# Optimization experiments

Hardware: AMD Instinct MI355X
Metric: run time of the kernel (lower is better)

Reference implementation:

```python
import jax, jax.numpy as jnp
import numpy as np

N, R, H, OUT = 512, 16, 16, 1
EPSILON = 1e-6
CUTOFF = 5.0  # ExpNormalSmearing cutoff_upper (cutoff_lower = 0)


def exp_normal_smearing(dist):
    # dist: (N, N, 1) -> (N, N, R); TorchMD-Net style ExpNormalSmearing
    start = jnp.exp(-CUTOFF)
    means = jnp.linspace(start, 1.0, R, dtype=dist.dtype)
    beta = (2.0 / R * (1.0 - start)) ** -2
    cutoff = 0.5 * (jnp.cos(dist * jnp.pi / CUTOFF) + 1.0) * (dist < CUTOFF)
    return cutoff * jnp.exp(-beta * (jnp.exp(-dist) - means) ** 2)


def setup_inputs() -> dict:
    key = jax.random.key(0)
    ks = jax.random.split(key, 9)
    s_in = 1.0 / np.sqrt(H * H)
    s_h = 1.0 / np.sqrt(H)
    return {
        "x": jax.random.normal(ks[0], (N, 3), jnp.float32) * 1.5,
        "W": jax.random.normal(ks[1], (2, N, R, H), jnp.float32) * 0.1,
        "W1": jax.random.normal(ks[2], (H, H * H), jnp.float32) * s_in,
        "b1": jax.random.normal(ks[3], (H,), jnp.float32) * 0.01,
        "W2": jax.random.normal(ks[4], (4 * R * H, H), jnp.float32) * s_h,
        "W3": jax.random.normal(ks[5], (H, H * H), jnp.float32) * s_in,
        "b3": jax.random.normal(ks[6], (H,), jnp.float32) * 0.01,
        "W4": jax.random.normal(ks[7], (OUT, H), jnp.float32) * s_h,
        "b4": jax.random.normal(ks[8], (OUT,), jnp.float32) * 0.01,
    }


def reference(x, W, W1, b1, W2, W3, b3, W4, b4):
    K, Q = W[0], W[1]                               # (N, R, H) each
    diff = x[:, None, :] - x[None, :, :]            # (N, N, 3)
    nsq = jnp.sum(diff * diff, axis=-1, keepdims=True) + EPSILON
    norm = jnp.sqrt(nsq)                            # (N, N, 1)
    diff = diff / nsq                               # note: divided by squared norm (faithful)
    sm = exp_normal_smearing(norm)                  # (N, N, R)
    basis = sm[..., None] * diff[..., None, :]      # (N, N, R, 3)

    bk = jnp.einsum('ijrb,jrc->icb', basis, K)      # (N, H, 3)
    bq = jnp.einsum('ijrb,jrc->icb', basis, Q)
    att = jnp.einsum('ihb,igb->ihg', bk, bq).reshape(N, H * H)
    att = jax.nn.silu(att @ W1.T + b1) @ W2.T       # (N, 4*R*H), second Linear bias-free

    left, right = att[:, : 2 * R * H], att[:, 2 * R * H:]
    pair = left[:, None, :] + right[None, :, :]     # (N, N, 2*R*H)
    K2 = pair[..., : R * H].reshape(N, N, R, H)
    Q2 = pair[..., R * H:].reshape(N, N, R, H)

    bk = jnp.einsum('ijrb,ijrc->icb', basis, K2)    # (N, H, 3)
    bq = jnp.einsum('ijrb,ijrc->icb', basis, Q2)
    att = jnp.einsum('ihb,igb->ihg', bk, bq).reshape(N, H * H)
    return jax.nn.silu(att @ W3.T + b3) @ W4.T + b4  # (N, OUT)
```

## Files before the change

### kernel.cpp

```cpp
#include <hip/hip_runtime.h>
#include <hip/hip_bf16.h>
#include <math.h>

#define NN 512

#define START 0.006737946999085467f
#define STEP  ((1.0f - START) * (1.0f/15.0f))
#define SB    (0.125f * (1.0f - START))
#define BETA  (1.0f/(SB*SB))
#define LOG2E 1.4426950408889634f
#define NB    (-(BETA)*LOG2E)


__global__ __launch_bounds__(256) void k0(const float* __restrict__ W,
                                          float* __restrict__ Wt)
{
    __shared__ float ldsb[256];
    const int row = blockIdx.x;
    ldsb[threadIdx.x] = W[(size_t)row*256 + threadIdx.x];
    __syncthreads();
    const int c = threadIdx.x >> 4, r = threadIdx.x & 15;
    Wt[(size_t)row*256 + threadIdx.x] = ldsb[r*16 + c];
}

__global__ __launch_bounds__(256) void k1a(const float* __restrict__ x,
                                           const float* __restrict__ Wt,
                                           float* __restrict__ part1)
{
    const int ib = blockIdx.x & 127, jc = blockIdx.x >> 7;
    const int i0 = ib * 4;
    const int tid = threadIdx.x;
    const int c = tid & 15, js = tid >> 4;
    const int lane = tid & 63, wv = tid >> 6;

    __shared__ float  lG[4][64][16];
    __shared__ float4 lP[4][64];
    __shared__ float  s_part[4][16][26];

    {
        const int pi = tid >> 6, pj = tid & 63;
        const int jg = jc*64 + pj;
        const float xi0 = x[(i0+pi)*3+0], xi1 = x[(i0+pi)*3+1], xi2 = x[(i0+pi)*3+2];
        float d0 = xi0 - x[jg*3+0];
        float d1 = xi1 - x[jg*3+1];
        float d2 = xi2 - x[jg*3+2];
        float nsq = fmaf(d0,d0, fmaf(d1,d1, fmaf(d2,d2, 1e-6f)));
        float rs  = __builtin_amdgcn_rsqf(nsq);
        float nrm = nsq * rs;
        float inv = rs * rs;
        float cutv = 0.f;
        if (nrm < 5.0f) cutv = 0.5f*(__cosf(nrm*0.6283185307179586f)+1.0f);
        float en = exp2f(-LOG2E * nrm);
        lP[pi][pj] = make_float4(d0*inv, d1*inv, d2*inv, 0.f);
        float4* dst = reinterpret_cast<float4*>(&lG[pi][pj][0]);
        #pragma unroll
        for (int rq = 0; rq < 4; ++rq) {
            float t0 = en - (START + STEP*(float)(4*rq+0));
            float t1 = en - (START + STEP*(float)(4*rq+1));
            float t2 = en - (START + STEP*(float)(4*rq+2));
            float t3 = en - (START + STEP*(float)(4*rq+3));
            dst[rq] = make_float4(cutv*exp2f(NB*t0*t0), cutv*exp2f(NB*t1*t1),
                                  cutv*exp2f(NB*t2*t2), cutv*exp2f(NB*t3*t3));
        }
    }
    __syncthreads();

    float acc[24];
    #pragma unroll
    for (int v = 0; v < 24; ++v) acc[v] = 0.f;

    #pragma unroll 1
    for (int t = 0; t < 4; ++t) {
        const int jl = js + 16*t;
        const int jg = jc*64 + jl;
        const float4* Kp = reinterpret_cast<const float4*>(Wt + (size_t)jg*256 + c*16);
        const float4* Qp = reinterpret_cast<const float4*>(Wt + (size_t)NN*256 + (size_t)jg*256 + c*16);
        float4 ka = Kp[0], kb = Kp[1], kc = Kp[2], kd = Kp[3];
        float4 qa = Qp[0], qb = Qp[1], qc = Qp[2], qd = Qp[3];

        #pragma unroll
        for (int i = 0; i < 4; ++i) {
            const float4* gp = reinterpret_cast<const float4*>(&lG[i][jl][0]);
            float4 g0 = gp[0], g1 = gp[1], g2 = gp[2], g3 = gp[3];
            float tk, tq;
            tk = g0.x*ka.x; tq = g0.x*qa.x;
            tk = fmaf(g0.y,ka.y,tk); tq = fmaf(g0.y,qa.y,tq);
            tk = fmaf(g0.z,ka.z,tk); tq = fmaf(g0.z,qa.z,tq);
            tk = fmaf(g0.w,ka.w,tk); tq = fmaf(g0.w,qa.w,tq);
            tk = fmaf(g1.x,kb.x,tk); tq = fmaf(g1.x,qb.x,tq);
            tk = fmaf(g1.y,kb.y,tk); tq = fmaf(g1.y,qb.y,tq);
            tk = fmaf(g1.z,kb.z,tk); tq = fmaf(g1.z,qb.z,tq);
            tk = fmaf(g1.w,kb.w,tk); tq = fmaf(g1.w,qb.w,tq);
            tk = fmaf(g2.x,kc.x,tk); tq = fmaf(g2.x,qc.x,tq);
            tk = fmaf(g2.y,kc.y,tk); tq = fmaf(g2.y,qc.y,tq);
            tk = fmaf(g2.z,kc.z,tk); tq = fmaf(g2.z,qc.z,tq);
            tk = fmaf(g2.w,kc.w,tk); tq = fmaf(g2.w,qc.w,tq);
            tk = fmaf(g3.x,kd.x,tk); tq = fmaf(g3.x,qd.x,tq);
            tk = fmaf(g3.y,kd.y,tk); tq = fmaf(g3.y,qd.y,tq);
            tk = fmaf(g3.z,kd.z,tk); tq = fmaf(g3.z,qd.z,tq);
            tk = fmaf(g3.w,kd.w,tk); tq = fmaf(g3.w,qd.w,tq);
            float4 dd = lP[i][jl];
            acc[i*6+0] = fmaf(tk, dd.x, acc[i*6+0]);
            acc[i*6+1] = fmaf(tk, dd.y, acc[i*6+1]);
            acc[i*6+2] = fmaf(tk, dd.z, acc[i*6+2]);
            acc[i*6+3] = fmaf(tq, dd.x, acc[i*6+3]);
            acc[i*6+4] = fmaf(tq, dd.y, acc[i*6+4]);
            acc[i*6+5] = fmaf(tq, dd.z, acc[i*6+5]);
        }
    }

    #pragma unroll
    for (int v = 0; v < 24; ++v) {
        float t = acc[v];
        t += __shfl_xor(t, 16);
        t += __shfl_xor(t, 32);
        if (lane < 16) s_part[wv][c][v] = t;
    }
    __syncthreads();

    for (int v = tid; v < 384; v += 256) {
        int i = v / 96, o = v - i*96;
        int kq = o / 48, rem = o - kq*48;
        int b = rem >> 4, c2 = rem & 15;
        int f = i*6 + kq*3 + b;
        float sum = s_part[0][c2][f] + s_part[1][c2][f]
                  + s_part[2][c2][f] + s_part[3][c2][f];
        part1[(i0+i)*768 + jc*96 + o] = sum;
    }
}

__global__ __launch_bounds__(256) void k1b(const float* __restrict__ part1,
                                           const float* __restrict__ W1,
                                           const float* __restrict__ b1,
                                           const float* __restrict__ W2,
                                           float* __restrict__ att2t)
{
    const int i = blockIdx.x;
    const int tid = threadIdx.x;
    __shared__ float s_bkq[96];
    __shared__ float s_att[256];
    __shared__ float s_z[16][16];
    __shared__ float s_a1[16];

    if (tid < 96) {
        const float* p = part1 + i*768 + tid;
        float s = 0.f;
        #pragma unroll
        for (int k = 0; k < 8; ++k) s += p[k*96];
        s_bkq[tid] = s;
    }
    __syncthreads();

    {
        int h = tid >> 4, g = tid & 15;
        s_att[tid] = s_bkq[     h]*s_bkq[48+     g]
                   + s_bkq[16 + h]*s_bkq[48+16 + g]
                   + s_bkq[32 + h]*s_bkq[48+32 + g];
    }
    __syncthreads();

    {
        int h = tid & 15, seg = tid >> 4;
        const float* w1 = W1 + h*256 + seg*16;
        const float* a  = s_att + seg*16;
        float p = 0.f;
        #pragma unroll
        for (int k = 0; k < 16; ++k) p = fmaf(a[k], w1[k], p);
        s_z[seg][h] = p;
    }
    __syncthreads();

    if (tid < 16) {
        float z = b1[tid];
        #pragma unroll
        for (int seg = 0; seg < 16; ++seg) z += s_z[seg][tid];
        s_a1[tid] = z / (1.0f + __expf(-z));
    }
    __syncthreads();

    float a1[16];
    #pragma unroll
    for (int cc = 0; cc < 16; ++cc) a1[cc] = s_a1[cc];
    #pragma unroll
    for (int p = 0; p < 4; ++p) {
        int o = tid + p*256;
        const float4* w2 = reinterpret_cast<const float4*>(W2 + o*16);
        float4 wa = w2[0], wb = w2[1], wc = w2[2], wd = w2[3];
        float accv = wa.x*a1[0] + wa.y*a1[1] + wa.z*a1[2] + wa.w*a1[3]
                   + wb.x*a1[4] + wb.y*a1[5] + wb.z*a1[6] + wb.w*a1[7]
                   + wc.x*a1[8] + wc.y*a1[9] + wc.z*a1[10]+ wc.w*a1[11]
                   + wd.x*a1[12]+ wd.y*a1[13]+ wd.z*a1[14]+ wd.w*a1[15];
        att2t[i*1024 + ((o>>8)*256) + ((o&15)*16) + ((o>>4)&15)] = accv;
    }
}

__global__ __launch_bounds__(256) void k2a(const float* __restrict__ x,
                                           const float* __restrict__ att2t,
                                           float* __restrict__ part2)
{
    const int ib = blockIdx.x & 127, jc = blockIdx.x >> 7;
    const int i0 = ib * 4;
    const int tid = threadIdx.x;
    const int c = tid & 15, js = tid >> 4;
    const int lane = tid & 63, wv = tid >> 6;

    __shared__ float  lG[4][64][16];
    __shared__ float4 lP[4][64];
    __shared__ float  s_part[4][16][38];

    {
        const int pi = tid >> 6, pj = tid & 63;
        const int jg = jc*64 + pj;
        const float xi0 = x[(i0+pi)*3+0], xi1 = x[(i0+pi)*3+1], xi2 = x[(i0+pi)*3+2];
        float d0 = xi0 - x[jg*3+0];
        float d1 = xi1 - x[jg*3+1];
        float d2 = xi2 - x[jg*3+2];
        float nsq = fmaf(d0,d0, fmaf(d1,d1, fmaf(d2,d2, 1e-6f)));
        float rs  = __builtin_amdgcn_rsqf(nsq);
        float nrm = nsq * rs;
        float inv = rs * rs;
        float cutv = 0.f;
        if (nrm < 5.0f) cutv = 0.5f*(__cosf(nrm*0.6283185307179586f)+1.0f);
        float en = exp2f(-LOG2E * nrm);
        lP[pi][pj] = make_float4(d0*inv, d1*inv, d2*inv, 0.f);
        float4* dst = reinterpret_cast<float4*>(&lG[pi][pj][0]);
        #pragma unroll
        for (int rq = 0; rq < 4; ++rq) {
            float t0 = en - (START + STEP*(float)(4*rq+0));
            float t1 = en - (START + STEP*(float)(4*rq+1));
            float t2 = en - (START + STEP*(float)(4*rq+2));
            float t3 = en - (START + STEP*(float)(4*rq+3));
            dst[rq] = make_float4(cutv*exp2f(NB*t0*t0), cutv*exp2f(NB*t1*t1),
                                  cutv*exp2f(NB*t2*t2), cutv*exp2f(NB*t3*t3));
        }
    }
    __syncthreads();

    float acc[36];
    #pragma unroll
    for (int v = 0; v < 36; ++v) acc[v] = 0.f;

    #pragma unroll 1
    for (int t = 0; t < 4; ++t) {
        const int jl = js + 16*t;
        const int jg = jc*64 + jl;
        const float4* Kp = reinterpret_cast<const float4*>(att2t + (size_t)jg*1024 + 512 + c*16);
        const float4* Qp = reinterpret_cast<const float4*>(att2t + (size_t)jg*1024 + 768 + c*16);
        float4 ka = Kp[0], kb = Kp[1], kc = Kp[2], kd = Kp[3];
        float4 qa = Qp[0], qb = Qp[1], qc = Qp[2], qd = Qp[3];

        #pragma unroll
        for (int i = 0; i < 4; ++i) {
            const float4* gp = reinterpret_cast<const float4*>(&lG[i][jl][0]);
            float4 g0 = gp[0], g1 = gp[1], g2 = gp[2], g3 = gp[3];
            float tk, tq;
            tk = g0.x*ka.x; tq = g0.x*qa.x;
            tk = fmaf(g0.y,ka.y,tk); tq = fmaf(g0.y,qa.y,tq);
            tk = fmaf(g0.z,ka.z,tk); tq = fmaf(g0.z,qa.z,tq);
            tk = fmaf(g0.w,ka.w,tk); tq = fmaf(g0.w,qa.w,tq);
            tk = fmaf(g1.x,kb.x,tk); tq = fmaf(g1.x,qb.x,tq);
            tk = fmaf(g1.y,kb.y,tk); tq = fmaf(g1.y,qb.y,tq);
            tk = fmaf(g1.z,kb.z,tk); tq = fmaf(g1.z,qb.z,tq);
            tk = fmaf(g1.w,kb.w,tk); tq = fmaf(g1.w,qb.w,tq);
            tk = fmaf(g2.x,kc.x,tk); tq = fmaf(g2.x,qc.x,tq);
            tk = fmaf(g2.y,kc.y,tk); tq = fmaf(g2.y,qc.y,tq);
            tk = fmaf(g2.z,kc.z,tk); tq = fmaf(g2.z,qc.z,tq);
            tk = fmaf(g2.w,kc.w,tk); tq = fmaf(g2.w,qc.w,tq);
            tk = fmaf(g3.x,kd.x,tk); tq = fmaf(g3.x,qd.x,tq);
            tk = fmaf(g3.y,kd.y,tk); tq = fmaf(g3.y,qd.y,tq);
            tk = fmaf(g3.z,kd.z,tk); tq = fmaf(g3.z,qd.z,tq);
            tk = fmaf(g3.w,kd.w,tk); tq = fmaf(g3.w,qd.w,tq);
            float4 dd = lP[i][jl];
            acc[i*6+0] = fmaf(tk, dd.x, acc[i*6+0]);
            acc[i*6+1] = fmaf(tk, dd.y, acc[i*6+1]);
            acc[i*6+2] = fmaf(tk, dd.z, acc[i*6+2]);
            acc[i*6+3] = fmaf(tq, dd.x, acc[i*6+3]);
            acc[i*6+4] = fmaf(tq, dd.y, acc[i*6+4]);
            acc[i*6+5] = fmaf(tq, dd.z, acc[i*6+5]);
            float gc = lG[i][jl][c];
            acc[24+i*3+0] = fmaf(gc, dd.x, acc[24+i*3+0]);
            acc[24+i*3+1] = fmaf(gc, dd.y, acc[24+i*3+1]);
            acc[24+i*3+2] = fmaf(gc, dd.z, acc[24+i*3+2]);
        }
    }

    #pragma unroll
    for (int v = 0; v < 36; ++v) {
        float t = acc[v];
        t += __shfl_xor(t, 16);
        t += __shfl_xor(t, 32);
        if (lane < 16) s_part[wv][c][v] = t;
    }
    __syncthreads();

    for (int v = tid; v < 576; v += 256) {
        int i = v / 144, o = v - i*144;
        int c2, f;
        if (o < 96) {
            int kq = o / 48, rem = o - kq*48;
            int b = rem >> 4; c2 = rem & 15;
            f = i*6 + kq*3 + b;
        } else {
            int oS = o - 96;
            int r = oS / 3, b = oS - r*3;
            c2 = r;
            f = 24 + i*3 + b;
        }
        float sum = s_part[0][c2][f] + s_part[1][c2][f]
                  + s_part[2][c2][f] + s_part[3][c2][f];
        part2[(i0+i)*1152 + jc*144 + o] = sum;
    }
}

__global__ __launch_bounds__(256) void k2b(const float* __restrict__ att2t,
                                           const float* __restrict__ part2,
                                           const float* __restrict__ W3,
                                           const float* __restrict__ b3,
                                           const float* __restrict__ W4,
                                           const float* __restrict__ b4,
                                           float* __restrict__ out)
{
    const int i = blockIdx.x;
    const int tid = threadIdx.x;
    __shared__ float s_red[144];
    __shared__ float s_att[256];
    __shared__ float s_z[16][16];
    __shared__ float s_a1[16];

    if (tid < 144) {
        const float* p = part2 + i*1152 + tid;
        float s = 0.f;
        #pragma unroll
        for (int k = 0; k < 8; ++k) s += p[k*144];
        s_red[tid] = s;
    }
    __syncthreads();

    if (tid < 96) {
        int kq = tid / 48, rem = tid - kq*48;
        int b = rem >> 4, cc = rem & 15;
        const float4* lrow = reinterpret_cast<const float4*>(att2t + i*1024 + kq*256 + cc*16);
        float4 A = lrow[0], B = lrow[1], C = lrow[2], D = lrow[3];
        float add = 0.f;
        add = fmaf(A.x, s_red[96+ 0*3+b], add);
        add = fmaf(A.y, s_red[96+ 1*3+b], add);
        add = fmaf(A.z, s_red[96+ 2*3+b], add);
        add = fmaf(A.w, s_red[96+ 3*3+b], add);
        add = fmaf(B.x, s_red[96+ 4*3+b], add);
        add = fmaf(B.y, s_red[96+ 5*3+b], add);
        add = fmaf(B.z, s_red[96+ 6*3+b], add);
        add = fmaf(B.w, s_red[96+ 7*3+b], add);
        add = fmaf(C.x, s_red[96+ 8*3+b], add);
        add = fmaf(C.y, s_red[96+ 9*3+b], add);
        add = fmaf(C.z, s_red[96+10*3+b], add);
        add = fmaf(C.w, s_red[96+11*3+b], add);
        add = fmaf(D.x, s_red[96+12*3+b], add);
        add = fmaf(D.y, s_red[96+13*3+b], add);
        add = fmaf(D.z, s_red[96+14*3+b], add);
        add = fmaf(D.w, s_red[96+15*3+b], add);
        s_red[tid] += add;
    }
    __syncthreads();

    {
        int h = tid >> 4, g = tid & 15;
        s_att[tid] = s_red[     h]*s_red[48+     g]
                   + s_red[16 + h]*s_red[48+16 + g]
                   + s_red[32 + h]*s_red[48+32 + g];
    }
    __syncthreads();

    {
        int h = tid & 15, seg = tid >> 4;
        const float* w3 = W3 + h*256 + seg*16;
        const float* a  = s_att + seg*16;
        float p = 0.f;
        #pragma unroll
        for (int k = 0; k < 16; ++k) p = fmaf(a[k], w3[k], p);
        s_z[seg][h] = p;
    }
    __syncthreads();

    if (tid < 16) {
        float z = b3[tid];
        #pragma unroll
        for (int seg = 0; seg < 16; ++seg) z += s_z[seg][tid];
        s_a1[tid] = z / (1.0f + __expf(-z));
    }
    __syncthreads();

    if (tid == 0) {
        float accv = b4[0];
        #pragma unroll
        for (int cc = 0; cc < 16; ++cc) accv = fmaf(s_a1[cc], W4[cc], accv);
        out[i] = accv;
    }
}

extern "C" void kernel_launch(void* const* d_in, const int* in_sizes, int n_in,
                              void* d_out, int out_size, void* d_ws, size_t ws_size,
                              hipStream_t stream) {
    (void)in_sizes; (void)n_in; (void)out_size; (void)ws_size;
    const float* x  = (const float*)d_in[0];
    const float* W  = (const float*)d_in[1];
    const float* W1 = (const float*)d_in[2];
    const float* b1 = (const float*)d_in[3];
    const float* W2 = (const float*)d_in[4];
    const float* W3 = (const float*)d_in[5];
    const float* b3 = (const float*)d_in[6];
    const float* W4 = (const float*)d_in[7];
    const float* b4 = (const float*)d_in[8];

    float* att2t = (float*)d_ws;
    float* part1 = att2t + 512*1024;
    float* part2 = part1 + 512*768;
    float* Wt    = part2 + 512*1152;
    float* out   = (float*)d_out;

    k0 <<<1024, 256, 0, stream>>>(W, Wt);
    k1a<<<1024, 256, 0, stream>>>(x, Wt, part1);
    k1b<<< 512, 256, 0, stream>>>(part1, W1, b1, W2, att2t);
    k2a<<<1024, 256, 0, stream>>>(x, att2t, part2);
    k2b<<< 512, 256, 0, stream>>>(att2t, part2, W3, b3, W4, b4, out);
}
```

Before: 118.2 us.

## Fuse five kernels into one persistent kernel with software grid barriers

Replaces the five separate launches (weight transpose, two pairwise accumulation stages, two per-row MLP stages) with one 512-block kernel that separates phases with atomic-counter grid barriers. Each block now handles two j-chunks, reusing the smearing basis it computes into a double-sized LDS buffer, and software-prefetches the next K/Q weight rows. The aim is to remove launch gaps and tail effects between small kernels. In exchange it halves the block count, raises LDS use, adds a memset launch, and depends on all 512 blocks being co-resident for the spin barrier to avoid deadlock.

```diff
diff --git a/kernel.cpp b/kernel.cpp
--- a/kernel.cpp
+++ b/kernel.cpp
@@ -1,8 +1,8 @@
 #include <hip/hip_runtime.h>
-#include <hip/hip_bf16.h>
 #include <math.h>
 
-#define NN 512
+#define NN   512
+#define NBLK 512
 
 #define START 0.006737946999085467f
 #define STEP  ((1.0f - START) * (1.0f/15.0f))
@@ -12,388 +12,375 @@
 #define NB    (-(BETA)*LOG2E)
 
 
-__global__ __launch_bounds__(256) void k0(const float* __restrict__ W,
-                                          float* __restrict__ Wt)
+__device__ __forceinline__ void gbar(unsigned* cnt, int k)
 {
-    __shared__ float ldsb[256];
-    const int row = blockIdx.x;
-    ldsb[threadIdx.x] = W[(size_t)row*256 + threadIdx.x];
     __syncthreads();
-    const int c = threadIdx.x >> 4, r = threadIdx.x & 15;
-    Wt[(size_t)row*256 + threadIdx.x] = ldsb[r*16 + c];
+    if (threadIdx.x == 0) {
+        __threadfence();
+        __hip_atomic_fetch_add(&cnt[k], 1u, __ATOMIC_RELEASE, __HIP_MEMORY_SCOPE_AGENT);
+        while (__hip_atomic_load(&cnt[k], __ATOMIC_RELAXED, __HIP_MEMORY_SCOPE_AGENT) < (unsigned)NBLK)
+            __builtin_amdgcn_s_sleep(8);
+        __threadfence();
+    }
+    __syncthreads();
 }
 
-__global__ __launch_bounds__(256) void k1a(const float* __restrict__ x,
-                                           const float* __restrict__ Wt,
-                                           float* __restrict__ part1)
+__device__ __forceinline__ void dot16(
+    float4 g0, float4 g1, float4 g2, float4 g3,
+    float4 ka, float4 kb, float4 kc, float4 kd,
+    float4 qa, float4 qb, float4 qc, float4 qd,
+    float& tk, float& tq)
 {
-    const int ib = blockIdx.x & 127, jc = blockIdx.x >> 7;
-    const int i0 = ib * 4;
+    tk = g0.x*ka.x; tq = g0.x*qa.x;
+    tk = fmaf(g0.y,ka.y,tk); tq = fmaf(g0.y,qa.y,tq);
+    tk = fmaf(g0.z,ka.z,tk); tq = fmaf(g0.z,qa.z,tq);
+    tk = fmaf(g0.w,ka.w,tk); tq = fmaf(g0.w,qa.w,tq);
+    tk = fmaf(g1.x,kb.x,tk); tq = fmaf(g1.x,qb.x,tq);
+    tk = fmaf(g1.y,kb.y,tk); tq = fmaf(g1.y,qb.y,tq);
+    tk = fmaf(g1.z,kb.z,tk); tq = fmaf(g1.z,qb.z,tq);
+    tk = fmaf(g1.w,kb.w,tk); tq = fmaf(g1.w,qb.w,tq);
+    tk = fmaf(g2.x,kc.x,tk); tq = fmaf(g2.x,qc.x,tq);
+    tk = fmaf(g2.y,kc.y,tk); tq = fmaf(g2.y,qc.y,tq);
+    tk = fmaf(g2.z,kc.z,tk); tq = fmaf(g2.z,qc.z,tq);
+    tk = fmaf(g2.w,kc.w,tk); tq = fmaf(g2.w,qc.w,tq);
+    tk = fmaf(g3.x,kd.x,tk); tq = fmaf(g3.x,qd.x,tq);
+    tk = fmaf(g3.y,kd.y,tk); tq = fmaf(g3.y,qd.y,tq);
+    tk = fmaf(g3.z,kd.z,tk); tq = fmaf(g3.z,qd.z,tq);
+    tk = fmaf(g3.w,kd.w,tk); tq = fmaf(g3.w,qd.w,tq);
+}
+
+__global__ __launch_bounds__(256) void mega(
+    const float* __restrict__ x,
+    const float* __restrict__ W,
+    const float* __restrict__ W1,
+    const float* __restrict__ b1,
+    const float* __restrict__ W2,
+    const float* __restrict__ W3,
+    const float* __restrict__ b3,
+    const float* __restrict__ W4,
+    const float* __restrict__ b4,
+    float* __restrict__ Wt,
+    float* __restrict__ part1,
+    float* __restrict__ part2,
+    float* __restrict__ att2t,
+    float* __restrict__ out,
+    unsigned* __restrict__ cnt)
+{
+    __shared__ __align__(16) float  lG[2][4][64][16];
+    __shared__ float4               lP[2][4][64];
+    __shared__ float                s_part[4][16][38];
+    __shared__ float                s_red[144];
+    __shared__ float                s_att[256];
+    __shared__ float                s_z[16][16];
+    __shared__ float                s_a1[16];
+
+    const int bid = blockIdx.x;
     const int tid = threadIdx.x;
-    const int c = tid & 15, js = tid >> 4;
+
+    #pragma unroll
+    for (int h = 0; h < 2; ++h) {
+        const int row = bid + h*512;
+        s_att[tid] = W[(size_t)row*256 + tid];
+        __syncthreads();
+        const int tc = tid >> 4, tr = tid & 15;
+        Wt[(size_t)row*256 + tid] = s_att[tr*16 + tc];
+        __syncthreads();
+    }
+    gbar(cnt, 0);
+
+    const int ib  = bid & 127, jcb = bid >> 7;
+    const int i0  = ib * 4;
+    const int c   = tid & 15, js = tid >> 4;
     const int lane = tid & 63, wv = tid >> 6;
-
-    __shared__ float  lG[4][64][16];
-    __shared__ float4 lP[4][64];
-    __shared__ float  s_part[4][16][26];
 
     {
         const int pi = tid >> 6, pj = tid & 63;
-        const int jg = jc*64 + pj;
         const float xi0 = x[(i0+pi)*3+0], xi1 = x[(i0+pi)*3+1], xi2 = x[(i0+pi)*3+2];
-        float d0 = xi0 - x[jg*3+0];
-        float d1 = xi1 - x[jg*3+1];
-        float d2 = xi2 - x[jg*3+2];
-        float nsq = fmaf(d0,d0, fmaf(d1,d1, fmaf(d2,d2, 1e-6f)));
-        float rs  = __builtin_amdgcn_rsqf(nsq);
-        float nrm = nsq * rs;
-        float inv = rs * rs;
-        float cutv = 0.f;
-        if (nrm < 5.0f) cutv = 0.5f*(__cosf(nrm*0.6283185307179586f)+1.0f);
-        float en = exp2f(-LOG2E * nrm);
-        lP[pi][pj] = make_float4(d0*inv, d1*inv, d2*inv, 0.f);
-        float4* dst = reinterpret_cast<float4*>(&lG[pi][pj][0]);
-        #pragma unroll
-        for (int rq = 0; rq < 4; ++rq) {
-            float t0 = en - (START + STEP*(float)(4*rq+0));
-            float t1 = en - (START + STEP*(float)(4*rq+1));
-            float t2 = en - (START + STEP*(float)(4*rq+2));
-            float t3 = en - (START + STEP*(float)(4*rq+3));
-            dst[rq] = make_float4(cutv*exp2f(NB*t0*t0), cutv*exp2f(NB*t1*t1),
-                                  cutv*exp2f(NB*t2*t2), cutv*exp2f(NB*t3*t3));
+        #pragma unroll
+        for (int un = 0; un < 2; ++un) {
+            const int jg = (jcb + 4*un)*64 + pj;
+            float d0 = xi0 - x[jg*3+0];
+            float d1 = xi1 - x[jg*3+1];
+            float d2 = xi2 - x[jg*3+2];
+            float nsq = fmaf(d0,d0, fmaf(d1,d1, fmaf(d2,d2, 1e-6f)));
+            float rs  = __builtin_amdgcn_rsqf(nsq);
+            float nrm = nsq * rs;
+            float inv = rs * rs;
+            float cutv = 0.f;
+            if (nrm < 5.0f) cutv = 0.5f*(__cosf(nrm*0.6283185307179586f)+1.0f);
+            float en = exp2f(-LOG2E * nrm);
+            lP[un][pi][pj] = make_float4(d0*inv, d1*inv, d2*inv, 0.f);
+            float4* dst = reinterpret_cast<float4*>(&lG[un][pi][pj][0]);
+            #pragma unroll
+            for (int rq = 0; rq < 4; ++rq) {
+                float t0 = en - (START + STEP*(float)(4*rq+0));
+                float t1 = en - (START + STEP*(float)(4*rq+1));
+                float t2 = en - (START + STEP*(float)(4*rq+2));
+                float t3 = en - (START + STEP*(float)(4*rq+3));
+                dst[rq] = make_float4(cutv*exp2f(NB*t0*t0), cutv*exp2f(NB*t1*t1),
+                                      cutv*exp2f(NB*t2*t2), cutv*exp2f(NB*t3*t3));
+            }
         }
     }
     __syncthreads();
 
-    float acc[24];
-    #pragma unroll
-    for (int v = 0; v < 24; ++v) acc[v] = 0.f;
-
     #pragma unroll 1
-    for (int t = 0; t < 4; ++t) {
-        const int jl = js + 16*t;
-        const int jg = jc*64 + jl;
-        const float4* Kp = reinterpret_cast<const float4*>(Wt + (size_t)jg*256 + c*16);
-        const float4* Qp = reinterpret_cast<const float4*>(Wt + (size_t)NN*256 + (size_t)jg*256 + c*16);
+    for (int un = 0; un < 2; ++un) {
+        const int jc = jcb + 4*un;
+        float acc[24];
+        #pragma unroll
+        for (int v = 0; v < 24; ++v) acc[v] = 0.f;
+
+        const float4* Kp = reinterpret_cast<const float4*>(Wt + (size_t)(jc*64 + js)*256 + c*16);
+        const float4* Qp = reinterpret_cast<const float4*>(Wt + (size_t)NN*256 + (size_t)(jc*64 + js)*256 + c*16);
         float4 ka = Kp[0], kb = Kp[1], kc = Kp[2], kd = Kp[3];
         float4 qa = Qp[0], qb = Qp[1], qc = Qp[2], qd = Qp[3];
 
-        #pragma unroll
-        for (int i = 0; i < 4; ++i) {
-            const float4* gp = reinterpret_cast<const float4*>(&lG[i][jl][0]);
-            float4 g0 = gp[0], g1 = gp[1], g2 = gp[2], g3 = gp[3];
-            float tk, tq;
-            tk = g0.x*ka.x; tq = g0.x*qa.x;
-            tk = fmaf(g0.y,ka.y,tk); tq = fmaf(g0.y,qa.y,tq);
-            tk = fmaf(g0.z,ka.z,tk); tq = fmaf(g0.z,qa.z,tq);
-            tk = fmaf(g0.w,ka.w,tk); tq = fmaf(g0.w,qa.w,tq);
-            tk = fmaf(g1.x,kb.x,tk); tq = fmaf(g1.x,qb.x,tq);
-            tk = fmaf(g1.y,kb.y,tk); tq = fmaf(g1.y,qb.y,tq);
-            tk = fmaf(g1.z,kb.z,tk); tq = fmaf(g1.z,qb.z,tq);
-            tk = fmaf(g1.w,kb.w,tk); tq = fmaf(g1.w,qb.w,tq);
-            tk = fmaf(g2.x,kc.x,tk); tq = fmaf(g2.x,qc.x,tq);
-            tk = fmaf(g2.y,kc.y,tk); tq = fmaf(g2.y,qc.y,tq);
-            tk = fmaf(g2.z,kc.z,tk); tq = fmaf(g2.z,qc.z,tq);
-            tk = fmaf(g2.w,kc.w,tk); tq = fmaf(g2.w,qc.w,tq);
-            tk = fmaf(g3.x,kd.x,tk); tq = fmaf(g3.x,qd.x,tq);
-            tk = fmaf(g3.y,kd.y,tk); tq = fmaf(g3.y,qd.y,tq);
-            tk = fmaf(g3.z,kd.z,tk); tq = fmaf(g3.z,qd.z,tq);
-            tk = fmaf(g3.w,kd.w,tk); tq = fmaf(g3.w,qd.w,tq);
-            float4 dd = lP[i][jl];
-            acc[i*6+0] = fmaf(tk, dd.x, acc[i*6+0]);
-            acc[i*6+1] = fmaf(tk, dd.y, acc[i*6+1]);
-            acc[i*6+2] = fmaf(tk, dd.z, acc[i*6+2]);
-            acc[i*6+3] = fmaf(tq, dd.x, acc[i*6+3]);
-            acc[i*6+4] = fmaf(tq, dd.y, acc[i*6+4]);
-            acc[i*6+5] = fmaf(tq, dd.z, acc[i*6+5]);
-        }
-    }
-
-    #pragma unroll
-    for (int v = 0; v < 24; ++v) {
-        float t = acc[v];
-        t += __shfl_xor(t, 16);
-        t += __shfl_xor(t, 32);
-        if (lane < 16) s_part[wv][c][v] = t;
-    }
-    __syncthreads();
-
-    for (int v = tid; v < 384; v += 256) {
-        int i = v / 96, o = v - i*96;
-        int kq = o / 48, rem = o - kq*48;
-        int b = rem >> 4, c2 = rem & 15;
-        int f = i*6 + kq*3 + b;
-        float sum = s_part[0][c2][f] + s_part[1][c2][f]
-                  + s_part[2][c2][f] + s_part[3][c2][f];
-        part1[(i0+i)*768 + jc*96 + o] = sum;
-    }
-}
-
-__global__ __launch_bounds__(256) void k1b(const float* __restrict__ part1,
-                                           const float* __restrict__ W1,
-                                           const float* __restrict__ b1,
-                                           const float* __restrict__ W2,
-                                           float* __restrict__ att2t)
-{
-    const int i = blockIdx.x;
-    const int tid = threadIdx.x;
-    __shared__ float s_bkq[96];
-    __shared__ float s_att[256];
-    __shared__ float s_z[16][16];
-    __shared__ float s_a1[16];
-
-    if (tid < 96) {
-        const float* p = part1 + i*768 + tid;
-        float s = 0.f;
-        #pragma unroll
-        for (int k = 0; k < 8; ++k) s += p[k*96];
-        s_bkq[tid] = s;
-    }
-    __syncthreads();
+        #pragma unroll 1
+        for (int t = 0; t < 4; ++t) {
+            float4 nka, nkb, nkc, nkd, nqa, nqb, nqc, nqd;
+            if (t < 3) {
+                const float4* Kn = Kp + (size_t)(t+1)*16*64;
+                const float4* Qn = Qp + (size_t)(t+1)*16*64;
+                nka = Kn[0]; nkb = Kn[1]; nkc = Kn[2]; nkd = Kn[3];
+                nqa = Qn[0]; nqb = Qn[1]; nqc = Qn[2]; nqd = Qn[3];
+            }
+            const int jl = js + 16*t;
+            #pragma unroll
+            for (int i = 0; i < 4; ++i) {
+                const float4* gp = reinterpret_cast<const float4*>(&lG[un][i][jl][0]);
+                float tk, tq;
+                dot16(gp[0], gp[1], gp[2], gp[3], ka,kb,kc,kd, qa,qb,qc,qd, tk, tq);
+                float4 dd = lP[un][i][jl];
+                acc[i*6+0] = fmaf(tk, dd.x, acc[i*6+0]);
+                acc[i*6+1] = fmaf(tk, dd.y, acc[i*6+1]);
+                acc[i*6+2] = fmaf(tk, dd.z, acc[i*6+2]);
+                acc[i*6+3] = fmaf(tq, dd.x, acc[i*6+3]);
+                acc[i*6+4] = fmaf(tq, dd.y, acc[i*6+4]);
+                acc[i*6+5] = fmaf(tq, dd.z, acc[i*6+5]);
+            }
+            if (t < 3) { ka=nka; kb=nkb; kc=nkc; kd=nkd; qa=nqa; qb=nqb; qc=nqc; qd=nqd; }
+        }
+
+        #pragma unroll
+        for (int v = 0; v < 24; ++v) {
+            float t2 = acc[v];
+            t2 += __shfl_xor(t2, 16);
+            t2 += __shfl_xor(t2, 32);
+            if (lane < 16) s_part[wv][c][v] = t2;
+        }
+        __syncthreads();
+
+        for (int v = tid; v < 384; v += 256) {
+            int i = v / 96, o = v - i*96;
+            int kq = o / 48, rem = o - kq*48;
+            int b = rem >> 4, c2 = rem & 15;
+            int f = i*6 + kq*3 + b;
+            float sum = s_part[0][c2][f] + s_part[1][c2][f]
+                      + s_part[2][c2][f] + s_part[3][c2][f];
+            part1[(i0+i)*768 + jc*96 + o] = sum;
+        }
+        __syncthreads();
+    }
+    gbar(cnt, 1);
 
     {
-        int h = tid >> 4, g = tid & 15;
-        s_att[tid] = s_bkq[     h]*s_bkq[48+     g]
-                   + s_bkq[16 + h]*s_bkq[48+16 + g]
-                   + s_bkq[32 + h]*s_bkq[48+32 + g];
-    }
-    __syncthreads();
-
-    {
-        int h = tid & 15, seg = tid >> 4;
-        const float* w1 = W1 + h*256 + seg*16;
-        const float* a  = s_att + seg*16;
-        float p = 0.f;
-        #pragma unroll
-        for (int k = 0; k < 16; ++k) p = fmaf(a[k], w1[k], p);
-        s_z[seg][h] = p;
-    }
-    __syncthreads();
-
-    if (tid < 16) {
-        float z = b1[tid];
-        #pragma unroll
-        for (int seg = 0; seg < 16; ++seg) z += s_z[seg][tid];
-        s_a1[tid] = z / (1.0f + __expf(-z));
-    }
-    __syncthreads();
-
-    float a1[16];
-    #pragma unroll
-    for (int cc = 0; cc < 16; ++cc) a1[cc] = s_a1[cc];
-    #pragma unroll
-    for (int p = 0; p < 4; ++p) {
-        int o = tid + p*256;
-        const float4* w2 = reinterpret_cast<const float4*>(W2 + o*16);
-        float4 wa = w2[0], wb = w2[1], wc = w2[2], wd = w2[3];
-        float accv = wa.x*a1[0] + wa.y*a1[1] + wa.z*a1[2] + wa.w*a1[3]
-                   + wb.x*a1[4] + wb.y*a1[5] + wb.z*a1[6] + wb.w*a1[7]
-                   + wc.x*a1[8] + wc.y*a1[9] + wc.z*a1[10]+ wc.w*a1[11]
-                   + wd.x*a1[12]+ wd.y*a1[13]+ wd.z*a1[14]+ wd.w*a1[15];
-        att2t[i*1024 + ((o>>8)*256) + ((o&15)*16) + ((o>>4)&15)] = accv;
-    }
-}
-
-__global__ __launch_bounds__(256) void k2a(const float* __restrict__ x,
-                                           const float* __restrict__ att2t,
-                                           float* __restrict__ part2)
-{
-    const int ib = blockIdx.x & 127, jc = blockIdx.x >> 7;
-    const int i0 = ib * 4;
-    const int tid = threadIdx.x;
-    const int c = tid & 15, js = tid >> 4;
-    const int lane = tid & 63, wv = tid >> 6;
-
-    __shared__ float  lG[4][64][16];
-    __shared__ float4 lP[4][64];
-    __shared__ float  s_part[4][16][38];
-
-    {
-        const int pi = tid >> 6, pj = tid & 63;
-        const int jg = jc*64 + pj;
-        const float xi0 = x[(i0+pi)*3+0], xi1 = x[(i0+pi)*3+1], xi2 = x[(i0+pi)*3+2];
-        float d0 = xi0 - x[jg*3+0];
-        float d1 = xi1 - x[jg*3+1];
-        float d2 = xi2 - x[jg*3+2];
-        float nsq = fmaf(d0,d0, fmaf(d1,d1, fmaf(d2,d2, 1e-6f)));
-        float rs  = __builtin_amdgcn_rsqf(nsq);
-        float nrm = nsq * rs;
-        float inv = rs * rs;
-        float cutv = 0.f;
-        if (nrm < 5.0f) cutv = 0.5f*(__cosf(nrm*0.6283185307179586f)+1.0f);
-        float en = exp2f(-LOG2E * nrm);
-        lP[pi][pj] = make_float4(d0*inv, d1*inv, d2*inv, 0.f);
-        float4* dst = reinterpret_cast<float4*>(&lG[pi][pj][0]);
-        #pragma unroll
-        for (int rq = 0; rq < 4; ++rq) {
-            float t0 = en - (START + STEP*(float)(4*rq+0));
-            float t1 = en - (START + STEP*(float)(4*rq+1));
-            float t2 = en - (START + STEP*(float)(4*rq+2));
-            float t3 = en - (START + STEP*(float)(4*rq+3));
-            dst[rq] = make_float4(cutv*exp2f(NB*t0*t0), cutv*exp2f(NB*t1*t1),
-                                  cutv*exp2f(NB*t2*t2), cutv*exp2f(NB*t3*t3));
-        }
-    }
-    __syncthreads();
-
-    float acc[36];
-    #pragma unroll
-    for (int v = 0; v < 36; ++v) acc[v] = 0.f;
+        const int i = bid;
+        if (tid < 96) {
+            const float* p = part1 + i*768 + tid;
+            float s = 0.f;
+            #pragma unroll
+            for (int k = 0; k < 8; ++k) s += p[k*96];
+            s_red[tid] = s;
+        }
+        __syncthreads();
+
+        {
+            int h = tid >> 4, g = tid & 15;
+            s_att[tid] = s_red[     h]*s_red[48+     g]
+                       + s_red[16 + h]*s_red[48+16 + g]
+                       + s_red[32 + h]*s_red[48+32 + g];
+        }
+        __syncthreads();
+
+        {
+            int h = tid & 15, seg = tid >> 4;
+            const float* w1 = W1 + h*256 + seg*16;
+            const float* a  = s_att + seg*16;
+            float p = 0.f;
+            #pragma unroll
+            for (int k = 0; k < 16; ++k) p = fmaf(a[k], w1[k], p);
+            s_z[seg][h] = p;
+        }
+        __syncthreads();
+
+        if (tid < 16) {
+            float z = b1[tid];
+            #pragma unroll
+            for (int seg = 0; seg < 16; ++seg) z += s_z[seg][tid];
+            s_a1[tid] = z / (1.0f + __expf(-z));
+        }
+        __syncthreads();
+
+        float a1[16];
+        #pragma unroll
+        for (int cc = 0; cc < 16; ++cc) a1[cc] = s_a1[cc];
+        #pragma unroll
+        for (int p = 0; p < 4; ++p) {
+            int o = tid + p*256;
+            const float4* w2 = reinterpret_cast<const float4*>(W2 + o*16);
+            float4 wa = w2[0], wb = w2[1], wc = w2[2], wd = w2[3];
+            float accv = wa.x*a1[0] + wa.y*a1[1] + wa.z*a1[2] + wa.w*a1[3]
+                       + wb.x*a1[4] + wb.y*a1[5] + wb.z*a1[6] + wb.w*a1[7]
+                       + wc.x*a1[8] + wc.y*a1[9] + wc.z*a1[10]+ wc.w*a1[11]
+                       + wd.x*a1[12]+ wd.y*a1[13]+ wd.z*a1[14]+ wd.w*a1[15];
+            att2t[i*1024 + ((o>>8)*256) + ((o&15)*16) + ((o>>4)&15)] = accv;
+        }
+    }
+    gbar(cnt, 2);
 
     #pragma unroll 1
-    for (int t = 0; t < 4; ++t) {
-        const int jl = js + 16*t;
-        const int jg = jc*64 + jl;
-        const float4* Kp = reinterpret_cast<const float4*>(att2t + (size_t)jg*1024 + 512 + c*16);
-        const float4* Qp = reinterpret_cast<const float4*>(att2t + (size_t)jg*1024 + 768 + c*16);
+    for (int un = 0; un < 2; ++un) {
+        const int jc = jcb + 4*un;
+        float acc[36];
+        #pragma unroll
+        for (int v = 0; v < 36; ++v) acc[v] = 0.f;
+
+        const float4* Kp = reinterpret_cast<const float4*>(att2t + (size_t)(jc*64 + js)*1024 + 512 + c*16);
+        const float4* Qp = reinterpret_cast<const float4*>(att2t + (size_t)(jc*64 + js)*1024 + 768 + c*16);
         float4 ka = Kp[0], kb = Kp[1], kc = Kp[2], kd = Kp[3];
         float4 qa = Qp[0], qb = Qp[1], qc = Qp[2], qd = Qp[3];
 
-        #pragma unroll
-        for (int i = 0; i < 4; ++i) {
-            const float4* gp = reinterpret_cast<const float4*>(&lG[i][jl][0]);
-            float4 g0 = gp[0], g1 = gp[1], g2 = gp[2], g3 = gp[3];
-            float tk, tq;
-            tk = g0.x*ka.x; tq = g0.x*qa.x;
-            tk = fmaf(g0.y,ka.y,tk); tq = fmaf(g0.y,qa.y,tq);
-            tk = fmaf(g0.z,ka.z,tk); tq = fmaf(g0.z,qa.z,tq);
-            tk = fmaf(g0.w,ka.w,tk); tq = fmaf(g0.w,qa.w,tq);
-            tk = fmaf(g1.x,kb.x,tk); tq = fmaf(g1.x,qb.x,tq);
-            tk = fmaf(g1.y,kb.y,tk); tq = fmaf(g1.y,qb.y,tq);
-            tk = fmaf(g1.z,kb.z,tk); tq = fmaf(g1.z,qb.z,tq);
-            tk = fmaf(g1.w,kb.w,tk); tq = fmaf(g1.w,qb.w,tq);
-            tk = fmaf(g2.x,kc.x,tk); tq = fmaf(g2.x,qc.x,tq);
-            tk = fmaf(g2.y,kc.y,tk); tq = fmaf(g2.y,qc.y,tq);
-            tk = fmaf(g2.z,kc.z,tk); tq = fmaf(g2.z,qc.z,tq);
-            tk = fmaf(g2.w,kc.w,tk); tq = fmaf(g2.w,qc.w,tq);
-            tk = fmaf(g3.x,kd.x,tk); tq = fmaf(g3.x,qd.x,tq);
-            tk = fmaf(g3.y,kd.y,tk); tq = fmaf(g3.y,qd.y,tq);
-            tk = fmaf(g3.z,kd.z,tk); tq = fmaf(g3.z,qd.z,tq);
-            tk = fmaf(g3.w,kd.w,tk); tq = fmaf(g3.w,qd.w,tq);
-            float4 dd = lP[i][jl];
-            acc[i*6+0] = fmaf(tk, dd.x, acc[i*6+0]);
-            acc[i*6+1] = fmaf(tk, dd.y, acc[i*6+1]);
-            acc[i*6+2] = fmaf(tk, dd.z, acc[i*6+2]);
-            acc[i*6+3] = fmaf(tq, dd.x, acc[i*6+3]);
-            acc[i*6+4] = fmaf(tq, dd.y, acc[i*6+4]);
-            acc[i*6+5] = fmaf(tq, dd.z, acc[i*6+5]);
-            float gc = lG[i][jl][c];
-            acc[24+i*3+0] = fmaf(gc, dd.x, acc[24+i*3+0]);
-            acc[24+i*3+1] = fmaf(gc, dd.y, acc[24+i*3+1]);
-            acc[24+i*3+2] = fmaf(gc, dd.z, acc[24+i*3+2]);
-        }
-    }
-
-    #pragma unroll
-    for (int v = 0; v < 36; ++v) {
-        float t = acc[v];
-        t += __shfl_xor(t, 16);
-        t += __shfl_xor(t, 32);
-        if (lane < 16) s_part[wv][c][v] = t;
-    }
-    __syncthreads();
-
-    for (int v = tid; v < 576; v += 256) {
-        int i = v / 144, o = v - i*144;
-        int c2, f;
-        if (o < 96) {
-            int kq = o / 48, rem = o - kq*48;
-            int b = rem >> 4; c2 = rem & 15;
-            f = i*6 + kq*3 + b;
-        } else {
-            int oS = o - 96;
-            int r = oS / 3, b = oS - r*3;
-            c2 = r;
-            f = 24 + i*3 + b;
-        }
-        float sum = s_part[0][c2][f] + s_part[1][c2][f]
-                  + s_part[2][c2][f] + s_part[3][c2][f];
-        part2[(i0+i)*1152 + jc*144 + o] = sum;
-    }
-}
-
-__global__ __launch_bounds__(256) void k2b(const float* __restrict__ att2t,
-                                           const float* __restrict__ part2,
-                                           const float* __restrict__ W3,
-                                           const float* __restrict__ b3,
-                                           const float* __restrict__ W4,
-                                           const float* __restrict__ b4,
-                                           float* __restrict__ out)
-{
-    const int i = blockIdx.x;
-    const int tid = threadIdx.x;
-    __shared__ float s_red[144];
-    __shared__ float s_att[256];
-    __shared__ float s_z[16][16];
-    __shared__ float s_a1[16];
-
-    if (tid < 144) {
-        const float* p = part2 + i*1152 + tid;
-        float s = 0.f;
-        #pragma unroll
-        for (int k = 0; k < 8; ++k) s += p[k*144];
-        s_red[tid] = s;
-    }
-    __syncthreads();
-
-    if (tid < 96) {
-        int kq = tid / 48, rem = tid - kq*48;
-        int b = rem >> 4, cc = rem & 15;
-        const float4* lrow = reinterpret_cast<const float4*>(att2t + i*1024 + kq*256 + cc*16);
-        float4 A = lrow[0], B = lrow[1], C = lrow[2], D = lrow[3];
-        float add = 0.f;
-        add = fmaf(A.x, s_red[96+ 0*3+b], add);
-        add = fmaf(A.y, s_red[96+ 1*3+b], add);
-        add = fmaf(A.z, s_red[96+ 2*3+b], add);
-        add = fmaf(A.w, s_red[96+ 3*3+b], add);
-        add = fmaf(B.x, s_red[96+ 4*3+b], add);
-        add = fmaf(B.y, s_red[96+ 5*3+b], add);
-        add = fmaf(B.z, s_red[96+ 6*3+b], add);
-        add = fmaf(B.w, s_red[96+ 7*3+b], add);
-        add = fmaf(C.x, s_red[96+ 8*3+b], add);
-        add = fmaf(C.y, s_red[96+ 9*3+b], add);
-        add = fmaf(C.z, s_red[96+10*3+b], add);
-        add = fmaf(C.w, s_red[96+11*3+b], add);
-        add = fmaf(D.x, s_red[96+12*3+b], add);
-        add = fmaf(D.y, s_red[96+13*3+b], add);
-        add = fmaf(D.z, s_red[96+14*3+b], add);
-        add = fmaf(D.w, s_red[96+15*3+b], add);
-        s_red[tid] += add;
-    }
-    __syncthreads();
+        #pragma unroll 1
+        for (int t = 0; t < 4; ++t) {
+            float4 nka, nkb, nkc, nkd, nqa, nqb, nqc, nqd;
+            if (t < 3) {
+                const float4* Kn = Kp + (size_t)(t+1)*16*256;
+                const float4* Qn = Qp + (size_t)(t+1)*16*256;
+                nka = Kn[0]; nkb = Kn[1]; nkc = Kn[2]; nkd = Kn[3];
+                nqa = Qn[0]; nqb = Qn[1]; nqc = Qn[2]; nqd = Qn[3];
+            }
+            const int jl = js + 16*t;
+            #pragma unroll
+            for (int i = 0; i < 4; ++i) {
+                const float4* gp = reinterpret_cast<const float4*>(&lG[un][i][jl][0]);
+                float tk, tq;
+                dot16(gp[0], gp[1], gp[2], gp[3], ka,kb,kc,kd, qa,qb,qc,qd, tk, tq);
+                float4 dd = lP[un][i][jl];
+                acc[i*6+0] = fmaf(tk, dd.x, acc[i*6+0]);
+                acc[i*6+1] = fmaf(tk, dd.y, acc[i*6+1]);
+                acc[i*6+2] = fmaf(tk, dd.z, acc[i*6+2]);
+                acc[i*6+3] = fmaf(tq, dd.x, acc[i*6+3]);
+                acc[i*6+4] = fmaf(tq, dd.y, acc[i*6+4]);
+                acc[i*6+5] = fmaf(tq, dd.z, acc[i*6+5]);
+                float gc = lG[un][i][jl][c];
+                acc[24+i*3+0] = fmaf(gc, dd.x, acc[24+i*3+0]);
+                acc[24+i*3+1] = fmaf(gc, dd.y, acc[24+i*3+1]);
+                acc[24+i*3+2] = fmaf(gc, dd.z, acc[24+i*3+2]);
+            }
+            if (t < 3) { ka=nka; kb=nkb; kc=nkc; kd=nkd; qa=nqa; qb=nqb; qc=nqc; qd=nqd; }
+        }
+
+        #pragma unroll
+        for (int v = 0; v < 36; ++v) {
+            float t2 = acc[v];
+            t2 += __shfl_xor(t2, 16);
+            t2 += __shfl_xor(t2, 32);
+            if (lane < 16) s_part[wv][c][v] = t2;
+        }
+        __syncthreads();
+
+        for (int v = tid; v < 576; v += 256) {
+            int i = v / 144, o = v - i*144;
+            int c2, f;
+            if (o < 96) {
+                int kq = o / 48, rem = o - kq*48;
+                int b = rem >> 4; c2 = rem & 15;
+                f = i*6 + kq*3 + b;
+            } else {
+                int oS = o - 96;
+                int r = oS / 3, b = oS - r*3;
+                c2 = r;
+                f = 24 + i*3 + b;
+            }
+            float sum = s_part[0][c2][f] + s_part[1][c2][f]
+                      + s_part[2][c2][f] + s_part[3][c2][f];
+            part2[(i0+i)*1152 + jc*144 + o] = sum;
+        }
+        __syncthreads();
+    }
+    gbar(cnt, 3);
 
     {
-        int h = tid >> 4, g = tid & 15;
-        s_att[tid] = s_red[     h]*s_red[48+     g]
-                   + s_red[16 + h]*s_red[48+16 + g]
-                   + s_red[32 + h]*s_red[48+32 + g];
-    }
-    __syncthreads();
-
-    {
-        int h = tid & 15, seg = tid >> 4;
-        const float* w3 = W3 + h*256 + seg*16;
-        const float* a  = s_att + seg*16;
-        float p = 0.f;
-        #pragma unroll
-        for (int k = 0; k < 16; ++k) p = fmaf(a[k], w3[k], p);
-        s_z[seg][h] = p;
-    }
-    __syncthreads();
-
-    if (tid < 16) {
-        float z = b3[tid];
-        #pragma unroll
-        for (int seg = 0; seg < 16; ++seg) z += s_z[seg][tid];
-        s_a1[tid] = z / (1.0f + __expf(-z));
-    }
-    __syncthreads();
-
-    if (tid == 0) {
-        float accv = b4[0];
-        #pragma unroll
-        for (int cc = 0; cc < 16; ++cc) accv = fmaf(s_a1[cc], W4[cc], accv);
-        out[i] = accv;
+        const int i = bid;
+        if (tid < 144) {
+            const float* p = part2 + i*1152 + tid;
+            float s = 0.f;
+            #pragma unroll
+            for (int k = 0; k < 8; ++k) s += p[k*144];
+            s_red[tid] = s;
+        }
+        __syncthreads();
+
+        if (tid < 96) {
+            int kq = tid / 48, rem = tid - kq*48;
+            int b = rem >> 4, cc = rem & 15;
+            const float4* lrow = reinterpret_cast<const float4*>(att2t + i*1024 + kq*256 + cc*16);
+            float4 A = lrow[0], B = lrow[1], C = lrow[2], D = lrow[3];
+            float add = 0.f;
+            add = fmaf(A.x, s_red[96+ 0*3+b], add);
+            add = fmaf(A.y, s_red[96+ 1*3+b], add);
+            add = fmaf(A.z, s_red[96+ 2*3+b], add);
+            add = fmaf(A.w, s_red[96+ 3*3+b], add);
+            add = fmaf(B.x, s_red[96+ 4*3+b], add);
+            add = fmaf(B.y, s_red[96+ 5*3+b], add);
+            add = fmaf(B.z, s_red[96+ 6*3+b], add);
+            add = fmaf(B.w, s_red[96+ 7*3+b], add);
+            add = fmaf(C.x, s_red[96+ 8*3+b], add);
+            add = fmaf(C.y, s_red[96+ 9*3+b], add);
+            add = fmaf(C.z, s_red[96+10*3+b], add);
+            add = fmaf(C.w, s_red[96+11*3+b], add);
+            add = fmaf(D.x, s_red[96+12*3+b], add);
+            add = fmaf(D.y, s_red[96+13*3+b], add);
+            add = fmaf(D.z, s_red[96+14*3+b], add);
+            add = fmaf(D.w, s_red[96+15*3+b], add);
+            s_red[tid] += add;
+        }
+        __syncthreads();
+
+        {
+            int h = tid >> 4, g = tid & 15;
+            s_att[tid] = s_red[     h]*s_red[48+     g]
+                       + s_red[16 + h]*s_red[48+16 + g]
+                       + s_red[32 + h]*s_red[48+32 + g];
+        }
+        __syncthreads();
+
+        {
+            int h = tid & 15, seg = tid >> 4;
+            const float* w3 = W3 + h*256 + seg*16;
+            const float* a  = s_att + seg*16;
+            float p = 0.f;
+            #pragma unroll
+            for (int k = 0; k < 16; ++k) p = fmaf(a[k], w3[k], p);
+            s_z[seg][h] = p;
+        }
+        __syncthreads();
+
+        if (tid < 16) {
+            float z = b3[tid];
+            #pragma unroll
+            for (int seg = 0; seg < 16; ++seg) z += s_z[seg][tid];
+            s_a1[tid] = z / (1.0f + __expf(-z));
+        }
+        __syncthreads();
+
+        if (tid == 0) {
+            float accv = b4[0];
+            #pragma unroll
+            for (int cc = 0; cc < 16; ++cc) accv = fmaf(s_a1[cc], W4[cc], accv);
+            out[i] = accv;
+        }
     }
 }
 
@@ -415,11 +402,10 @@
     float* part1 = att2t + 512*1024;
     float* part2 = part1 + 512*768;
     float* Wt    = part2 + 512*1152;
+    unsigned* cnt = (unsigned*)(Wt + 2*512*256);
     float* out   = (float*)d_out;
 
-    k0 <<<1024, 256, 0, stream>>>(W, Wt);
-    k1a<<<1024, 256, 0, stream>>>(x, Wt, part1);
-    k1b<<< 512, 256, 0, stream>>>(part1, W1, b1, W2, att2t);
-    k2a<<<1024, 256, 0, stream>>>(x, att2t, part2);
-    k2b<<< 512, 256, 0, stream>>>(att2t, part2, W3, b3, W4, b4, out);
+    hipMemsetAsync(cnt, 0, 4*sizeof(unsigned), stream);
+    mega<<<NBLK, 256, 0, stream>>>(x, W, W1, b1, W2, W3, b3, W4, b4,
+                                   Wt, part1, part2, att2t, out, cnt);
 }
```

Result: slower. 306.0 us (+158.8%).
